# Kernel optimization log

Measured on AMD Instinct MI355X. Metric: run time of the kernel, lower is better.

The kernel has to match this reference:

```python
import jax, jax.numpy as jnp
import numpy as np

N = 100000
E = 1600000
IN_CH, HID_CH, OUT_CH, HEADS = 128, 32, 64, 4
NEG_SLOPE = 0.2


def gat_conv(x, src, dst, W, att_src, att_dst, bias, concat):
    """PyG-style GATConv (inference; dropout off). src/dst include self-loops.
    x: [N, Fin], W: [Fin, H*C], att_*: [H, C], bias: [H*C] or [C]."""
    n = x.shape[0]
    H, C = att_src.shape
    h = (x @ W).reshape(n, H, C)                      # [N, H, C]
    a_s = jnp.sum(h * att_src, axis=-1)               # [N, H]
    a_d = jnp.sum(h * att_dst, axis=-1)               # [N, H]
    e = jax.nn.leaky_relu(a_s[src] + a_d[dst], NEG_SLOPE)   # [E, H]
    # segment softmax over incoming edges of each dst node
    e_max = jax.ops.segment_max(e, dst, num_segments=n)     # [N, H]
    e_exp = jnp.exp(e - e_max[dst])                          # [E, H]
    denom = jax.ops.segment_sum(e_exp, dst, num_segments=n) # [N, H]
    alpha = e_exp / (denom[dst] + 1e-16)                     # [E, H]
    msg = h[src] * alpha[:, :, None]                         # [E, H, C]
    out = jax.ops.segment_sum(msg, dst, num_segments=n)     # [N, H, C]
    out = out.reshape(n, H * C) if concat else out.mean(axis=1)
    return out + bias


def setup_inputs() -> dict:
    key = jax.random.key(0)
    ks = jax.random.split(key, 10)
    g = 1.0 / np.sqrt(IN_CH)
    g2 = 1.0 / np.sqrt(HID_CH * HEADS)
    return {
        "x": jax.random.normal(ks[0], (N, IN_CH), dtype=jnp.float32),
        "edge_index": jax.random.randint(ks[1], (2, E), 0, N, dtype=jnp.int64),
        "W1": jax.random.normal(ks[2], (IN_CH, HEADS * HID_CH), dtype=jnp.float32) * g,
        "att_src1": jax.random.normal(ks[3], (HEADS, HID_CH), dtype=jnp.float32) * g,
        "att_dst1": jax.random.normal(ks[4], (HEADS, HID_CH), dtype=jnp.float32) * g,
        "b1": jnp.zeros((HEADS * HID_CH,), dtype=jnp.float32),
        "W2": jax.random.normal(ks[5], (HEADS * HID_CH, OUT_CH), dtype=jnp.float32) * g2,
        "att_src2": jax.random.normal(ks[6], (1, OUT_CH), dtype=jnp.float32) * g2,
        "att_dst2": jax.random.normal(ks[7], (1, OUT_CH), dtype=jnp.float32) * g2,
        "b2": jnp.zeros((OUT_CH,), dtype=jnp.float32),
    }


def reference(x, edge_index, W1, att_src1, att_dst1, b1, W2, att_src2, att_dst2, b2):
    n = x.shape[0]
    # GATConv adds self-loops by default (fixed-size concat: jit friendly)
    loops = jnp.arange(n, dtype=edge_index.dtype)
    src = jnp.concatenate([edge_index[0], loops])
    dst = jnp.concatenate([edge_index[1], loops])
    h = gat_conv(x, src, dst, W1, att_src1, att_dst1, b1, concat=True)
    h = jax.nn.elu(h)
    return gat_conv(h, src, dst, W2, att_src2, att_dst2, b2, concat=False)
```

## Files before the change

### kernel.cpp

```cpp
#include <hip/hip_runtime.h>
#include <hip/hip_fp16.h>

#define NEG_SLOPE 0.2f
#define BKN 128
#define MAXNB 1024
#define GRP 256
#define LOG2E 1.44269504f

typedef _Float16 half_t;
typedef __attribute__((ext_vector_type(2))) _Float16 half2v;
typedef __attribute__((ext_vector_type(4))) _Float16 half4;
typedef __attribute__((ext_vector_type(8))) _Float16 half8;
typedef __attribute__((ext_vector_type(4))) float floatx4;

#if __has_builtin(__builtin_amdgcn_fdot2)
#define FDOT2(a, b, c) __builtin_amdgcn_fdot2((a), (b), (c), false)
#else
#define FDOT2(a, b, c) ((float)(a)[0] * (float)(b)[0] + (float)(a)[1] * (float)(b)[1] + (c))
#endif

template<int BN, int HEADS, bool INHALF>
__global__ __launch_bounds__(256) void gemm_mfma(
    const void* __restrict__ Xv, const half_t* __restrict__ Wt,
    const float* __restrict__ atts, const float* __restrict__ attd,
    half_t* __restrict__ H, float* __restrict__ As, float* __restrict__ Ad,
    int n)
{
    constexpr int K  = 128;
    constexpr int NT = BN / 16;
    constexpr int TPH = NT / HEADS;

    __shared__ half_t Wl[BN * K];
    __shared__ half_t Xl[64 * K];

    const int t = threadIdx.x;
    const int wave = t >> 6, lane = t & 63;
    const int quad = lane >> 4, c = lane & 15;

    float att_s[NT], att_d[NT];
    #pragma unroll
    for (int nt = 0; nt < NT; ++nt) {
        att_s[nt] = atts[nt * 16 + c] * LOG2E;
        att_d[nt] = attd[nt * 16 + c] * LOG2E;
    }

    for (int i = t; i < BN * 16; i += 256) {
        int row = i >> 4, cid = i & 15;
        half8 v = *(const half8*)(Wt + row * K + cid * 8);
        *(half8*)(Wl + row * K + ((cid ^ (row & 15)) << 3)) = v;
    }

    const int numTiles = (n + 63) / 64;
    for (int tile = blockIdx.x; tile < numTiles; tile += gridDim.x) {
        const int row0 = tile * 64;
        __syncthreads();
        for (int i = t; i < 1024; i += 256) {
            int m = i >> 4, cid = i & 15;
            int row = row0 + m;
            half8 h;
            #pragma unroll
            for (int z = 0; z < 8; ++z) h[z] = (half_t)0.f;
            if (row < n) {
                if constexpr (INHALF) {
                    h = *(const half8*)((const half_t*)Xv + (size_t)row * K + cid * 8);
                } else {
                    const float4* src = (const float4*)((const float*)Xv + (size_t)row * K + cid * 8);
                    float4 a = src[0], b = src[1];
                    h[0]=(half_t)a.x; h[1]=(half_t)a.y; h[2]=(half_t)a.z; h[3]=(half_t)a.w;
                    h[4]=(half_t)b.x; h[5]=(half_t)b.y; h[6]=(half_t)b.z; h[7]=(half_t)b.w;
                }
            }
            *(half8*)(Xl + m * K + ((cid ^ (m & 15)) << 3)) = h;
        }
        __syncthreads();

        floatx4 acc[NT];
        #pragma unroll
        for (int i = 0; i < NT; ++i) acc[i] = (floatx4)(0.f);

        #pragma unroll
        for (int kc = 0; kc < 4; ++kc) {
            int cid = kc * 4 + quad;
            half8 afrag = *(const half8*)(Xl + (wave * 16 + c) * K + ((cid ^ c) << 3));
            #pragma unroll
            for (int nt = 0; nt < NT; ++nt) {
                half8 bfrag = *(const half8*)(Wl + (nt * 16 + c) * K + ((cid ^ c) << 3));
                acc[nt] = __builtin_amdgcn_mfma_f32_16x16x32_f16(afrag, bfrag, acc[nt], 0, 0, 0);
            }
        }

        #pragma unroll
        for (int reg = 0; reg < 4; ++reg) {
            int row = row0 + wave * 16 + quad * 4 + reg;
            bool ok = row < n;
            if (ok) {
                #pragma unroll
                for (int nt = 0; nt < NT; ++nt)
                    H[(size_t)row * BN + nt * 16 + c] = (half_t)acc[nt][reg];
            }
            #pragma unroll
            for (int h = 0; h < HEADS; ++h) {
                float ps = 0.f, pd = 0.f;
                #pragma unroll
                for (int u = 0; u < TPH; ++u) {
                    int nt = h * TPH + u;
                    ps += acc[nt][reg] * att_s[nt];
                    pd += acc[nt][reg] * att_d[nt];
                }
                #pragma unroll
                for (int off = 1; off < 16; off <<= 1) {
                    ps += __shfl_xor(ps, off);
                    pd += __shfl_xor(pd, off);
                }
                if (ok && c == 0) {
                    As[(size_t)row * HEADS + h] = ps;
                    Ad[(size_t)row * HEADS + h] = pd;
                }
            }
        }
    }
}

__global__ __launch_bounds__(256) void ghist_wconv(
    const int* __restrict__ ei, int E, int Etot, int NB, int chunk,
    int* __restrict__ cnt,
    const float* __restrict__ W1, half_t* __restrict__ Wt1,
    const float* __restrict__ W2, half_t* __restrict__ Wt2)
{
    int iw = blockIdx.x * 256 + threadIdx.x;
    if (iw < 128 * 128) {
        int k = iw / 128, nn = iw % 128;
        Wt1[nn * 128 + k] = (half_t)W1[iw];
    } else if (iw < 128 * 128 + 128 * 64) {
        int jx = iw - 128 * 128;
        int k = jx / 64, nn = jx % 64;
        Wt2[nn * 128 + k] = (half_t)W2[jx];
    }

    __shared__ int h[MAXNB];
    int g = blockIdx.x;
    for (int i = threadIdx.x; i < NB; i += 256) h[i] = 0;
    __syncthreads();
    int lo = g * chunk, hi = min(Etot, lo + chunk);
    for (int e = lo + threadIdx.x; e < hi; e += 256) {
        int dst = (e < E) ? ei[E + e] : (e - E);
        atomicAdd(&h[dst >> 7], 1);
    }
    __syncthreads();
    for (int i = threadIdx.x; i < NB; i += 256) cnt[i * GRP + g] = h[i];
}

__global__ __launch_bounds__(256) void scan_blocks(
    int* __restrict__ data, int n, int* __restrict__ bsum)
{
    __shared__ int s[256];
    int t = threadIdx.x;
    int idx = blockIdx.x * 1024 + t * 4;
    int4 v = make_int4(0, 0, 0, 0);
    if (idx + 3 < n)      v = *(const int4*)(data + idx);
    else {
        if (idx     < n) v.x = data[idx];
        if (idx + 1 < n) v.y = data[idx+1];
        if (idx + 2 < n) v.z = data[idx+2];
        if (idx + 3 < n) v.w = data[idx+3];
    }
    int tsum = v.x + v.y + v.z + v.w;
    s[t] = tsum;
    __syncthreads();
    for (int off = 1; off < 256; off <<= 1) {
        int x = (t >= off) ? s[t - off] : 0;
        __syncthreads();
        s[t] += x;
        __syncthreads();
    }
    int excl = s[t] - tsum;
    if (t == 255) bsum[blockIdx.x] = s[255];
    if (idx     < n) data[idx]     = excl;
    if (idx + 1 < n) data[idx + 1] = excl + v.x;
    if (idx + 2 < n) data[idx + 2] = excl + v.x + v.y;
    if (idx + 3 < n) data[idx + 3] = excl + v.x + v.y + v.z;
}

__global__ __launch_bounds__(256) void pass1_gemm1(
    const int* __restrict__ ei, int E, int Etot, int NB, int chunk, int nbC,
    const int* __restrict__ S, const int* __restrict__ bsum,
    unsigned* __restrict__ tmp,
    const float* __restrict__ X, const half_t* __restrict__ Wt,
    const float* __restrict__ atts, const float* __restrict__ attd,
    half_t* __restrict__ H, float* __restrict__ As, float* __restrict__ Ad,
    int n)
{
    constexpr int K = 128, BN = 128, NT = 8, HEADS = 4, TPH = 2;
    __shared__ half_t Wl[BN * K];
    __shared__ half_t Xl[64 * K];
    __shared__ int cur[MAXNB];

    const int t = threadIdx.x;

    if (blockIdx.x < GRP) {
        int* bs  = (int*)Wl;
        int* bse = (int*)Wl + 256;
        int g = blockIdx.x;
        int val = (t < nbC) ? bsum[t] : 0;
        bs[t] = val;
        __syncthreads();
        for (int off = 1; off < 256; off <<= 1) {
            int x = (t >= off) ? bs[t - off] : 0;
            __syncthreads();
            bs[t] += x;
            __syncthreads();
        }
        bse[t] = bs[t] - val;
        __syncthreads();
        for (int i = t; i < NB; i += 256) {
            int idx = i * GRP + g;
            cur[i] = S[idx] + bse[idx >> 10];
        }
        __syncthreads();
        int lo = g * chunk, hi = min(Etot, lo + chunk);
        for (int e = lo + t; e < hi; e += 256) {
            int src, dst;
            if (e < E) { src = ei[e]; dst = ei[E + e]; }
            else       { src = dst = e - E; }
            int pos = atomicAdd(&cur[dst >> 7], 1);
            tmp[pos] = ((unsigned)src << 7) | (unsigned)(dst & (BKN - 1));
        }
        return;
    }

    const int wave = t >> 6, lane = t & 63;
    const int quad = lane >> 4, c = lane & 15;

    float att_s[NT], att_d[NT];
    #pragma unroll
    for (int nt = 0; nt < NT; ++nt) {
        att_s[nt] = atts[nt * 16 + c] * LOG2E;
        att_d[nt] = attd[nt * 16 + c] * LOG2E;
    }

    for (int i = t; i < BN * 16; i += 256) {
        int row = i >> 4, cid = i & 15;
        half8 v = *(const half8*)(Wt + row * K + cid * 8);
        *(half8*)(Wl + row * K + ((cid ^ (row & 15)) << 3)) = v;
    }

    const int numTiles = (n + 63) / 64;
    for (int tile = blockIdx.x - GRP; tile < numTiles; tile += gridDim.x - GRP) {
        const int row0 = tile * 64;
        __syncthreads();
        for (int i = t; i < 1024; i += 256) {
            int m = i >> 4, cid = i & 15;
            int row = row0 + m;
            half8 h;
            #pragma unroll
            for (int z = 0; z < 8; ++z) h[z] = (half_t)0.f;
            if (row < n) {
                const float4* src = (const float4*)(X + (size_t)row * K + cid * 8);
                float4 a = src[0], b = src[1];
                h[0]=(half_t)a.x; h[1]=(half_t)a.y; h[2]=(half_t)a.z; h[3]=(half_t)a.w;
                h[4]=(half_t)b.x; h[5]=(half_t)b.y; h[6]=(half_t)b.z; h[7]=(half_t)b.w;
            }
            *(half8*)(Xl + m * K + ((cid ^ (m & 15)) << 3)) = h;
        }
        __syncthreads();

        floatx4 acc[NT];
        #pragma unroll
        for (int i = 0; i < NT; ++i) acc[i] = (floatx4)(0.f);

        #pragma unroll
        for (int kc = 0; kc < 4; ++kc) {
            int cid = kc * 4 + quad;
            half8 afrag = *(const half8*)(Xl + (wave * 16 + c) * K + ((cid ^ c) << 3));
            #pragma unroll
            for (int nt = 0; nt < NT; ++nt) {
                half8 bfrag = *(const half8*)(Wl + (nt * 16 + c) * K + ((cid ^ c) << 3));
                acc[nt] = __builtin_amdgcn_mfma_f32_16x16x32_f16(afrag, bfrag, acc[nt], 0, 0, 0);
            }
        }

        #pragma unroll
        for (int reg = 0; reg < 4; ++reg) {
            int row = row0 + wave * 16 + quad * 4 + reg;
            bool ok = row < n;
            if (ok) {
                #pragma unroll
                for (int nt = 0; nt < NT; ++nt)
                    H[(size_t)row * BN + nt * 16 + c] = (half_t)acc[nt][reg];
            }
            #pragma unroll
            for (int h = 0; h < HEADS; ++h) {
                float ps = 0.f, pd = 0.f;
                #pragma unroll
                for (int u = 0; u < TPH; ++u) {
                    int nt = h * TPH + u;
                    ps += acc[nt][reg] * att_s[nt];
                    pd += acc[nt][reg] * att_d[nt];
                }
                #pragma unroll
                for (int off = 1; off < 16; off <<= 1) {
                    ps += __shfl_xor(ps, off);
                    pd += __shfl_xor(pd, off);
                }
                if (ok && c == 0) {
                    As[(size_t)row * HEADS + h] = ps;
                    Ad[(size_t)row * HEADS + h] = pd;
                }
            }
        }
    }
}

__global__ __launch_bounds__(256) void pass2_sort(
    const unsigned* __restrict__ tmp, const int* __restrict__ S,
    const int* __restrict__ bsum, int NB, int Etot, int nbC,
    int* __restrict__ offs, int* __restrict__ esrc, int n)
{
    __shared__ int cnt[BKN];
    __shared__ int sc[BKN];
    __shared__ int cur[BKN];
    __shared__ int bs[256];
    __shared__ int bse[256];
    int bk = blockIdx.x;
    int t  = threadIdx.x;

    int val = (t < nbC) ? bsum[t] : 0;
    bs[t] = val;
    if (t < BKN) cnt[t] = 0;
    __syncthreads();
    for (int off = 1; off < 256; off <<= 1) {
        int x = (t >= off) ? bs[t - off] : 0;
        __syncthreads();
        bs[t] += x;
        __syncthreads();
    }
    bse[t] = bs[t] - val;
    __syncthreads();

    int lo = S[bk * GRP] + bse[(bk * GRP) >> 10];
    int hi = (bk + 1 < NB) ? (S[(bk + 1) * GRP] + bse[((bk + 1) * GRP) >> 10]) : Etot;

    for (int i = lo + t; i < hi; i += 256)
        atomicAdd(&cnt[tmp[i] & (BKN - 1)], 1);
    __syncthreads();
    int v = (t < BKN) ? cnt[t] : 0;
    if (t < BKN) sc[t] = v;
    __syncthreads();
    for (int off = 1; off < BKN; off <<= 1) {
        int x = (t < BKN && t >= off) ? sc[t - off] : 0;
        __syncthreads();
        if (t < BKN) sc[t] += x;
        __syncthreads();
    }
    if (t < BKN) {
        int node = bk * BKN + t;
        if (node < n) offs[node] = lo + sc[t];
        cur[t] = lo + sc[t] - v;
    }
    __syncthreads();
    for (int i = lo + t; i < hi; i += 256) {
        unsigned w = tmp[i];
        int p = atomicAdd(&cur[w & (BKN - 1)], 1);
        esrc[p] = (int)(w >> 7);
    }
}

__global__ __launch_bounds__(256) void agg1(
    const int* __restrict__ offs, const int* __restrict__ esrc,
    const half8* __restrict__ H8, const float* __restrict__ As,
    const float* __restrict__ Ad, const float* __restrict__ bias,
    half_t* __restrict__ X2h, int n)
{
    int v    = (blockIdx.x * 256 + threadIdx.x) >> 6;
    int lane = threadIdx.x & 63;
    if (v >= n) return;
    int q    = lane >> 4;
    int li   = lane & 15;
    int head = li >> 2;
    int end = offs[v];
    int beg = v ? offs[v - 1] : 0;
    float adv = Ad[(size_t)v * 4 + head];
    half2v one; one[0] = (half_t)1.f; one[1] = (half_t)1.f;
    float a[8];
    #pragma unroll
    for (int f = 0; f < 8; ++f) a[f] = 0.f;
    float den = 0.f;
    int j = beg + q;
    for (; j + 12 < end; j += 16) {
        int s0 = esrc[j], s1 = esrc[j + 4], s2 = esrc[j + 8], s3 = esrc[j + 12];
        float e0 = As[(unsigned)(s0 * 4 + head)] + adv;
        float e1 = As[(unsigned)(s1 * 4 + head)] + adv;
        float e2 = As[(unsigned)(s2 * 4 + head)] + adv;
        float e3 = As[(unsigned)(s3 * 4 + head)] + adv;
        half8 q0 = H8[(unsigned)(s0 * 16 + li)];
        half8 q1 = H8[(unsigned)(s1 * 16 + li)];
        half8 q2 = H8[(unsigned)(s2 * 16 + li)];
        half8 q3 = H8[(unsigned)(s3 * 16 + li)];
        float w0 = __builtin_amdgcn_exp2f(fmaxf(e0, NEG_SLOPE * e0));
        float w1 = __builtin_amdgcn_exp2f(fmaxf(e1, NEG_SLOPE * e1));
        float w2 = __builtin_amdgcn_exp2f(fmaxf(e2, NEG_SLOPE * e2));
        float w3 = __builtin_amdgcn_exp2f(fmaxf(e3, NEG_SLOPE * e3));
        half2v wp01; wp01[0] = (half_t)w0; wp01[1] = (half_t)w1;
        half2v wp23; wp23[0] = (half_t)w2; wp23[1] = (half_t)w3;
        #pragma unroll
        for (int f = 0; f < 8; ++f) {
            half2v p01; p01[0] = q0[f]; p01[1] = q1[f];
            half2v p23; p23[0] = q2[f]; p23[1] = q3[f];
            a[f] = FDOT2(p01, wp01, a[f]);
            a[f] = FDOT2(p23, wp23, a[f]);
        }
        den = FDOT2(wp01, one, den);
        den = FDOT2(wp23, one, den);
    }
    for (; j + 4 < end; j += 8) {
        int s0 = esrc[j], s1 = esrc[j + 4];
        float e0 = As[(unsigned)(s0 * 4 + head)] + adv;
        float e1 = As[(unsigned)(s1 * 4 + head)] + adv;
        half8 q0 = H8[(unsigned)(s0 * 16 + li)];
        half8 q1 = H8[(unsigned)(s1 * 16 + li)];
        float w0 = __builtin_amdgcn_exp2f(fmaxf(e0, NEG_SLOPE * e0));
        float w1 = __builtin_amdgcn_exp2f(fmaxf(e1, NEG_SLOPE * e1));
        half2v wp; wp[0] = (half_t)w0; wp[1] = (half_t)w1;
        #pragma unroll
        for (int f = 0; f < 8; ++f) {
            half2v p; p[0] = q0[f]; p[1] = q1[f];
            a[f] = FDOT2(p, wp, a[f]);
        }
        den = FDOT2(wp, one, den);
    }
    for (; j < end; j += 4) {
        int s = esrc[j];
        float e = As[(unsigned)(s * 4 + head)] + adv;
        half8 q0 = H8[(unsigned)(s * 16 + li)];
        float w = __builtin_amdgcn_exp2f(fmaxf(e, NEG_SLOPE * e));
        #pragma unroll
        for (int f = 0; f < 8; ++f) a[f] += w * (float)q0[f];
        den += w;
    }
    #pragma unroll
    for (int f = 0; f < 8; ++f) {
        a[f] += __shfl_xor(a[f], 16);
        a[f] += __shfl_xor(a[f], 32);
    }
    den += __shfl_xor(den, 16);
    den += __shfl_xor(den, 32);
    if (q == 0) {
        float inv = 1.f / (den + 1e-16f);
        float4 b0 = ((const float4*)bias)[2 * li];
        float4 b1 = ((const float4*)bias)[2 * li + 1];
        float o[8];
        o[0] = a[0] * inv + b0.x; o[1] = a[1] * inv + b0.y;
        o[2] = a[2] * inv + b0.z; o[3] = a[3] * inv + b0.w;
        o[4] = a[4] * inv + b1.x; o[5] = a[5] * inv + b1.y;
        o[6] = a[6] * inv + b1.z; o[7] = a[7] * inv + b1.w;
        half8 h;
        #pragma unroll
        for (int f = 0; f < 8; ++f) {
            float e = o[f] > 0.f ? o[f] : __expf(o[f]) - 1.f;
            h[f] = (half_t)e;
        }
        *(half8*)(X2h + (size_t)v * 128 + li * 8) = h;
    }
}

__global__ __launch_bounds__(256) void agg2(
    const int* __restrict__ offs, const int* __restrict__ esrc,
    const half8* __restrict__ H8, const float* __restrict__ As,
    const float* __restrict__ Ad, const float* __restrict__ bias,
    float* __restrict__ out, int n)
{
    int v    = (blockIdx.x * 256 + threadIdx.x) >> 6;
    int lane = threadIdx.x & 63;
    if (v >= n) return;
    int g  = lane >> 3;
    int li = lane & 7;
    int end = offs[v];
    int beg = v ? offs[v - 1] : 0;
    float adv = Ad[v];
    half2v one; one[0] = (half_t)1.f; one[1] = (half_t)1.f;
    float a[8];
    #pragma unroll
    for (int f = 0; f < 8; ++f) a[f] = 0.f;
    float den = 0.f;
    int j = beg + g;
    for (; j + 24 < end; j += 32) {
        int s0 = esrc[j], s1 = esrc[j + 8], s2 = esrc[j + 16], s3 = esrc[j + 24];
        float e0 = As[s0] + adv;
        float e1 = As[s1] + adv;
        float e2 = As[s2] + adv;
        float e3 = As[s3] + adv;
        half8 q0 = H8[(unsigned)(s0 * 8 + li)];
        half8 q1 = H8[(unsigned)(s1 * 8 + li)];
        half8 q2 = H8[(unsigned)(s2 * 8 + li)];
        half8 q3 = H8[(unsigned)(s3 * 8 + li)];
        float w0 = __builtin_amdgcn_exp2f(fmaxf(e0, NEG_SLOPE * e0));
        float w1 = __builtin_amdgcn_exp2f(fmaxf(e1, NEG_SLOPE * e1));
        float w2 = __builtin_amdgcn_exp2f(fmaxf(e2, NEG_SLOPE * e2));
        float w3 = __builtin_amdgcn_exp2f(fmaxf(e3, NEG_SLOPE * e3));
        half2v wp01; wp01[0] = (half_t)w0; wp01[1] = (half_t)w1;
        half2v wp23; wp23[0] = (half_t)w2; wp23[1] = (half_t)w3;
        #pragma unroll
        for (int f = 0; f < 8; ++f) {
            half2v p01; p01[0] = q0[f]; p01[1] = q1[f];
            half2v p23; p23[0] = q2[f]; p23[1] = q3[f];
            a[f] = FDOT2(p01, wp01, a[f]);
            a[f] = FDOT2(p23, wp23, a[f]);
        }
        den = FDOT2(wp01, one, den);
        den = FDOT2(wp23, one, den);
    }
    for (; j + 8 < end; j += 16) {
        int s0 = esrc[j], s1 = esrc[j + 8];
        float e0 = As[s0] + adv;
        float e1 = As[s1] + adv;
        half8 q0 = H8[(unsigned)(s0 * 8 + li)];
        half8 q1 = H8[(unsigned)(s1 * 8 + li)];
        float w0 = __builtin_amdgcn_exp2f(fmaxf(e0, NEG_SLOPE * e0));
        float w1 = __builtin_amdgcn_exp2f(fmaxf(e1, NEG_SLOPE * e1));
        half2v wp; wp[0] = (half_t)w0; wp[1] = (half_t)w1;
        #pragma unroll
        for (int f = 0; f < 8; ++f) {
            half2v p; p[0] = q0[f]; p[1] = q1[f];
            a[f] = FDOT2(p, wp, a[f]);
        }
        den = FDOT2(wp, one, den);
    }
    for (; j < end; j += 8) {
        int s = esrc[j];
        float e = As[s] + adv;
        half8 q0 = H8[(unsigned)(s * 8 + li)];
        float w = __builtin_amdgcn_exp2f(fmaxf(e, NEG_SLOPE * e));
        #pragma unroll
        for (int f = 0; f < 8; ++f) a[f] += w * (float)q0[f];
        den += w;
    }
    #pragma unroll
    for (int f = 0; f < 8; ++f) {
        a[f] += __shfl_xor(a[f], 8);
        a[f] += __shfl_xor(a[f], 16);
        a[f] += __shfl_xor(a[f], 32);
    }
    den += __shfl_xor(den, 8);
    den += __shfl_xor(den, 16);
    den += __shfl_xor(den, 32);
    if (lane < 8) {
        float inv = 1.f / (den + 1e-16f);
        float4 b0 = ((const float4*)bias)[2 * li];
        float4 b1 = ((const float4*)bias)[2 * li + 1];
        float4* o4 = (float4*)(out + (size_t)v * 64);
        o4[2 * li]     = make_float4(a[0] * inv + b0.x, a[1] * inv + b0.y,
                                     a[2] * inv + b0.z, a[3] * inv + b0.w);
        o4[2 * li + 1] = make_float4(a[4] * inv + b1.x, a[5] * inv + b1.y,
                                     a[6] * inv + b1.z, a[7] * inv + b1.w);
    }
}

extern "C" void kernel_launch(void* const* d_in, const int* in_sizes, int n_in,
                              void* d_out, int out_size, void* d_ws, size_t ws_size,
                              hipStream_t stream)
{
    (void)n_in; (void)out_size; (void)ws_size;
    const float* x   = (const float*)d_in[0];
    const int*   ei  = (const int*)  d_in[1];
    const float* W1  = (const float*)d_in[2];
    const float* as1 = (const float*)d_in[3];
    const float* ad1 = (const float*)d_in[4];
    const float* b1  = (const float*)d_in[5];
    const float* W2  = (const float*)d_in[6];
    const float* as2 = (const float*)d_in[7];
    const float* ad2 = (const float*)d_in[8];
    const float* b2  = (const float*)d_in[9];
    float* out = (float*)d_out;

    const int n    = in_sizes[0] / 128;
    const int E    = in_sizes[1] / 2;
    const int Etot = E + n;
    const int NB   = (n + BKN - 1) / BKN;
    const int chunk = (Etot + GRP - 1) / GRP;

    char* p = (char*)d_ws;
    half_t* Hh  = (half_t*)p; p += (size_t)n * 128 * sizeof(half_t);
    half_t* X2h = (half_t*)p; p += (size_t)n * 128 * sizeof(half_t);
    float* As1 = (float*)p;   p += (size_t)n * 4 * sizeof(float);
    float* Ad1 = (float*)p;   p += (size_t)n * 4 * sizeof(float);
    int* offs  = (int*)p;     p += (size_t)n * sizeof(int);
    int* esrc  = (int*)p;     p += (size_t)Etot * sizeof(int);
    unsigned* tmp = (unsigned*)p; p += (size_t)Etot * sizeof(unsigned);
    int* cnt   = (int*)p;     p += (size_t)NB * GRP * sizeof(int);
    int* bsum  = (int*)p;     p += 1024;
    half_t* Wt1 = (half_t*)p; p += 128 * 128 * sizeof(half_t);
    half_t* Wt2 = (half_t*)p; p += 64 * 128 * sizeof(half_t);

    const int scan_n  = NB * GRP;
    const int scan_nb = (scan_n + 1023) / 1024;

    const int gtiles = (n + 63) / 64;

    ghist_wconv<<<GRP, 256, 0, stream>>>(ei, E, Etot, NB, chunk, cnt, W1, Wt1, W2, Wt2);
    scan_blocks<<<scan_nb, 256, 0, stream>>>(cnt, scan_n, bsum);
    pass1_gemm1<<<GRP + gtiles, 256, 0, stream>>>(ei, E, Etot, NB, chunk, scan_nb, cnt, bsum, tmp,
                                                  x, Wt1, as1, ad1, Hh, As1, Ad1, n);
    pass2_sort<<<NB, 256, 0, stream>>>(tmp, cnt, bsum, NB, Etot, scan_nb, offs, esrc, n);

    agg1<<<(n * 64 + 255) / 256, 256, 0, stream>>>(offs, esrc, (const half8*)Hh, As1, Ad1, b1, X2h, n);

    gemm_mfma<64, 1, true><<<gtiles, 256, 0, stream>>>(X2h, Wt2, as2, ad2, Hh, As1, Ad1, n);
    agg2<<<(n * 64 + 255) / 256, 256, 0, stream>>>(offs, esrc, (const half8*)Hh, As1, Ad1, b2, out, n);
}
```

Measured before the change: 299.5 us.

## Fuse layer-2 projection and attention logits into layer-1 aggregation kernel

The layer-1 aggregation kernel now multiplies each node's ELU output by W2 in the same kernel, using fdot2 against a W2 copy staged in LDS, and writes H2 plus the layer-2 attention scalars directly. This removes the X2h intermediate round trip through global memory and the separate MFMA GEMM launch. The cost is a 64-wide-per-node dot product done with scalar fdot2 instead of MFMA, plus a 16KB LDS W2 load in every block, which may reduce occupancy. The unused templated gemm_mfma kernel is removed and the remaining kernels are reordered.

```diff
diff --git a/kernel.cpp b/kernel.cpp
--- a/kernel.cpp
+++ b/kernel.cpp
@@ -19,21 +19,113 @@
 #define FDOT2(a, b, c) ((float)(a)[0] * (float)(b)[0] + (float)(a)[1] * (float)(b)[1] + (c))
 #endif
 
-template<int BN, int HEADS, bool INHALF>
-__global__ __launch_bounds__(256) void gemm_mfma(
-    const void* __restrict__ Xv, const half_t* __restrict__ Wt,
+__global__ __launch_bounds__(256) void ghist_wconv(
+    const int* __restrict__ ei, int E, int Etot, int NB, int chunk,
+    int* __restrict__ cnt,
+    const float* __restrict__ W1, half_t* __restrict__ Wt1,
+    const float* __restrict__ W2, half_t* __restrict__ Wt2)
+{
+    int iw = blockIdx.x * 256 + threadIdx.x;
+    if (iw < 128 * 128) {
+        int k = iw / 128, nn = iw % 128;
+        Wt1[nn * 128 + k] = (half_t)W1[iw];
+    } else if (iw < 128 * 128 + 128 * 64) {
+        int jx = iw - 128 * 128;
+        int k = jx / 64, nn = jx % 64;
+        Wt2[nn * 128 + k] = (half_t)W2[jx];
+    }
+
+    __shared__ int h[MAXNB];
+    int g = blockIdx.x;
+    for (int i = threadIdx.x; i < NB; i += 256) h[i] = 0;
+    __syncthreads();
+    int lo = g * chunk, hi = min(Etot, lo + chunk);
+    for (int e = lo + threadIdx.x; e < hi; e += 256) {
+        int dst = (e < E) ? ei[E + e] : (e - E);
+        atomicAdd(&h[dst >> 7], 1);
+    }
+    __syncthreads();
+    for (int i = threadIdx.x; i < NB; i += 256) cnt[i * GRP + g] = h[i];
+}
+
+__global__ __launch_bounds__(256) void scan_blocks(
+    int* __restrict__ data, int n, int* __restrict__ bsum)
+{
+    __shared__ int s[256];
+    int t = threadIdx.x;
+    int idx = blockIdx.x * 1024 + t * 4;
+    int4 v = make_int4(0, 0, 0, 0);
+    if (idx + 3 < n)      v = *(const int4*)(data + idx);
+    else {
+        if (idx     < n) v.x = data[idx];
+        if (idx + 1 < n) v.y = data[idx+1];
+        if (idx + 2 < n) v.z = data[idx+2];
+        if (idx + 3 < n) v.w = data[idx+3];
+    }
+    int tsum = v.x + v.y + v.z + v.w;
+    s[t] = tsum;
+    __syncthreads();
+    for (int off = 1; off < 256; off <<= 1) {
+        int x = (t >= off) ? s[t - off] : 0;
+        __syncthreads();
+        s[t] += x;
+        __syncthreads();
+    }
+    int excl = s[t] - tsum;
+    if (t == 255) bsum[blockIdx.x] = s[255];
+    if (idx     < n) data[idx]     = excl;
+    if (idx + 1 < n) data[idx + 1] = excl + v.x;
+    if (idx + 2 < n) data[idx + 2] = excl + v.x + v.y;
+    if (idx + 3 < n) data[idx + 3] = excl + v.x + v.y + v.z;
+}
+
+__global__ __launch_bounds__(256) void pass1_gemm1(
+    const int* __restrict__ ei, int E, int Etot, int NB, int chunk, int nbC,
+    const int* __restrict__ S, const int* __restrict__ bsum,
+    unsigned* __restrict__ tmp,
+    const float* __restrict__ X, const half_t* __restrict__ Wt,
     const float* __restrict__ atts, const float* __restrict__ attd,
     half_t* __restrict__ H, float* __restrict__ As, float* __restrict__ Ad,
     int n)
 {
-    constexpr int K  = 128;
-    constexpr int NT = BN / 16;
-    constexpr int TPH = NT / HEADS;
-
+    constexpr int K = 128, BN = 128, NT = 8, HEADS = 4, TPH = 2;
     __shared__ half_t Wl[BN * K];
     __shared__ half_t Xl[64 * K];
+    __shared__ int cur[MAXNB];
 
     const int t = threadIdx.x;
+
+    if (blockIdx.x < GRP) {
+        int* bs  = (int*)Wl;
+        int* bse = (int*)Wl + 256;
+        int g = blockIdx.x;
+        int val = (t < nbC) ? bsum[t] : 0;
+        bs[t] = val;
+        __syncthreads();
+        for (int off = 1; off < 256; off <<= 1) {
+            int x = (t >= off) ? bs[t - off] : 0;
+            __syncthreads();
+            bs[t] += x;
+            __syncthreads();
+        }
+        bse[t] = bs[t] - val;
+        __syncthreads();
+        for (int i = t; i < NB; i += 256) {
+            int idx = i * GRP + g;
+            cur[i] = S[idx] + bse[idx >> 10];
+        }
+        __syncthreads();
+        int lo = g * chunk, hi = min(Etot, lo + chunk);
+        for (int e = lo + t; e < hi; e += 256) {
+            int src, dst;
+            if (e < E) { src = ei[e]; dst = ei[E + e]; }
+            else       { src = dst = e - E; }
+            int pos = atomicAdd(&cur[dst >> 7], 1);
+            tmp[pos] = ((unsigned)src << 7) | (unsigned)(dst & (BKN - 1));
+        }
+        return;
+    }
+
     const int wave = t >> 6, lane = t & 63;
     const int quad = lane >> 4, c = lane & 15;
 
@@ -51,7 +143,7 @@
     }
 
     const int numTiles = (n + 63) / 64;
-    for (int tile = blockIdx.x; tile < numTiles; tile += gridDim.x) {
+    for (int tile = blockIdx.x - GRP; tile < numTiles; tile += gridDim.x - GRP) {
         const int row0 = tile * 64;
         __syncthreads();
         for (int i = t; i < 1024; i += 256) {
@@ -61,14 +153,10 @@
             #pragma unroll
             for (int z = 0; z < 8; ++z) h[z] = (half_t)0.f;
             if (row < n) {
-                if constexpr (INHALF) {
-                    h = *(const half8*)((const half_t*)Xv + (size_t)row * K + cid * 8);
-                } else {
-                    const float4* src = (const float4*)((const float*)Xv + (size_t)row * K + cid * 8);
-                    float4 a = src[0], b = src[1];
-                    h[0]=(half_t)a.x; h[1]=(half_t)a.y; h[2]=(half_t)a.z; h[3]=(half_t)a.w;
-                    h[4]=(half_t)b.x; h[5]=(half_t)b.y; h[6]=(half_t)b.z; h[7]=(half_t)b.w;
-                }
+                const float4* src = (const float4*)(X + (size_t)row * K + cid * 8);
+                float4 a = src[0], b = src[1];
+                h[0]=(half_t)a.x; h[1]=(half_t)a.y; h[2]=(half_t)a.z; h[3]=(half_t)a.w;
+                h[4]=(half_t)b.x; h[5]=(half_t)b.y; h[6]=(half_t)b.z; h[7]=(half_t)b.w;
             }
             *(half8*)(Xl + m * K + ((cid ^ (m & 15)) << 3)) = h;
         }
@@ -121,196 +209,6 @@
     }
 }
 
-__global__ __launch_bounds__(256) void ghist_wconv(
-    const int* __restrict__ ei, int E, int Etot, int NB, int chunk,
-    int* __restrict__ cnt,
-    const float* __restrict__ W1, half_t* __restrict__ Wt1,
-    const float* __restrict__ W2, half_t* __restrict__ Wt2)
-{
-    int iw = blockIdx.x * 256 + threadIdx.x;
-    if (iw < 128 * 128) {
-        int k = iw / 128, nn = iw % 128;
-        Wt1[nn * 128 + k] = (half_t)W1[iw];
-    } else if (iw < 128 * 128 + 128 * 64) {
-        int jx = iw - 128 * 128;
-        int k = jx / 64, nn = jx % 64;
-        Wt2[nn * 128 + k] = (half_t)W2[jx];
-    }
-
-    __shared__ int h[MAXNB];
-    int g = blockIdx.x;
-    for (int i = threadIdx.x; i < NB; i += 256) h[i] = 0;
-    __syncthreads();
-    int lo = g * chunk, hi = min(Etot, lo + chunk);
-    for (int e = lo + threadIdx.x; e < hi; e += 256) {
-        int dst = (e < E) ? ei[E + e] : (e - E);
-        atomicAdd(&h[dst >> 7], 1);
-    }
-    __syncthreads();
-    for (int i = threadIdx.x; i < NB; i += 256) cnt[i * GRP + g] = h[i];
-}
-
-__global__ __launch_bounds__(256) void scan_blocks(
-    int* __restrict__ data, int n, int* __restrict__ bsum)
-{
-    __shared__ int s[256];
-    int t = threadIdx.x;
-    int idx = blockIdx.x * 1024 + t * 4;
-    int4 v = make_int4(0, 0, 0, 0);
-    if (idx + 3 < n)      v = *(const int4*)(data + idx);
-    else {
-        if (idx     < n) v.x = data[idx];
-        if (idx + 1 < n) v.y = data[idx+1];
-        if (idx + 2 < n) v.z = data[idx+2];
-        if (idx + 3 < n) v.w = data[idx+3];
-    }
-    int tsum = v.x + v.y + v.z + v.w;
-    s[t] = tsum;
-    __syncthreads();
-    for (int off = 1; off < 256; off <<= 1) {
-        int x = (t >= off) ? s[t - off] : 0;
-        __syncthreads();
-        s[t] += x;
-        __syncthreads();
-    }
-    int excl = s[t] - tsum;
-    if (t == 255) bsum[blockIdx.x] = s[255];
-    if (idx     < n) data[idx]     = excl;
-    if (idx + 1 < n) data[idx + 1] = excl + v.x;
-    if (idx + 2 < n) data[idx + 2] = excl + v.x + v.y;
-    if (idx + 3 < n) data[idx + 3] = excl + v.x + v.y + v.z;
-}
-
-__global__ __launch_bounds__(256) void pass1_gemm1(
-    const int* __restrict__ ei, int E, int Etot, int NB, int chunk, int nbC,
-    const int* __restrict__ S, const int* __restrict__ bsum,
-    unsigned* __restrict__ tmp,
-    const float* __restrict__ X, const half_t* __restrict__ Wt,
-    const float* __restrict__ atts, const float* __restrict__ attd,
-    half_t* __restrict__ H, float* __restrict__ As, float* __restrict__ Ad,
-    int n)
-{
-    constexpr int K = 128, BN = 128, NT = 8, HEADS = 4, TPH = 2;
-    __shared__ half_t Wl[BN * K];
-    __shared__ half_t Xl[64 * K];
-    __shared__ int cur[MAXNB];
-
-    const int t = threadIdx.x;
-
-    if (blockIdx.x < GRP) {
-        int* bs  = (int*)Wl;
-        int* bse = (int*)Wl + 256;
-        int g = blockIdx.x;
-        int val = (t < nbC) ? bsum[t] : 0;
-        bs[t] = val;
-        __syncthreads();
-        for (int off = 1; off < 256; off <<= 1) {
-            int x = (t >= off) ? bs[t - off] : 0;
-            __syncthreads();
-            bs[t] += x;
-            __syncthreads();
-        }
-        bse[t] = bs[t] - val;
-        __syncthreads();
-        for (int i = t; i < NB; i += 256) {
-            int idx = i * GRP + g;
-            cur[i] = S[idx] + bse[idx >> 10];
-        }
-        __syncthreads();
-        int lo = g * chunk, hi = min(Etot, lo + chunk);
-        for (int e = lo + t; e < hi; e += 256) {
-            int src, dst;
-            if (e < E) { src = ei[e]; dst = ei[E + e]; }
-            else       { src = dst = e - E; }
-            int pos = atomicAdd(&cur[dst >> 7], 1);
-            tmp[pos] = ((unsigned)src << 7) | (unsigned)(dst & (BKN - 1));
-        }
-        return;
-    }
-
-    const int wave = t >> 6, lane = t & 63;
-    const int quad = lane >> 4, c = lane & 15;
-
-    float att_s[NT], att_d[NT];
-    #pragma unroll
-    for (int nt = 0; nt < NT; ++nt) {
-        att_s[nt] = atts[nt * 16 + c] * LOG2E;
-        att_d[nt] = attd[nt * 16 + c] * LOG2E;
-    }
-
-    for (int i = t; i < BN * 16; i += 256) {
-        int row = i >> 4, cid = i & 15;
-        half8 v = *(const half8*)(Wt + row * K + cid * 8);
-        *(half8*)(Wl + row * K + ((cid ^ (row & 15)) << 3)) = v;
-    }
-
-    const int numTiles = (n + 63) / 64;
-    for (int tile = blockIdx.x - GRP; tile < numTiles; tile += gridDim.x - GRP) {
-        const int row0 = tile * 64;
-        __syncthreads();
-        for (int i = t; i < 1024; i += 256) {
-            int m = i >> 4, cid = i & 15;
-            int row = row0 + m;
-            half8 h;
-            #pragma unroll
-            for (int z = 0; z < 8; ++z) h[z] = (half_t)0.f;
-            if (row < n) {
-                const float4* src = (const float4*)(X + (size_t)row * K + cid * 8);
-                float4 a = src[0], b = src[1];
-                h[0]=(half_t)a.x; h[1]=(half_t)a.y; h[2]=(half_t)a.z; h[3]=(half_t)a.w;
-                h[4]=(half_t)b.x; h[5]=(half_t)b.y; h[6]=(half_t)b.z; h[7]=(half_t)b.w;
-            }
-            *(half8*)(Xl + m * K + ((cid ^ (m & 15)) << 3)) = h;
-        }
-        __syncthreads();
-
-        floatx4 acc[NT];
-        #pragma unroll
-        for (int i = 0; i < NT; ++i) acc[i] = (floatx4)(0.f);
-
-        #pragma unroll
-        for (int kc = 0; kc < 4; ++kc) {
-            int cid = kc * 4 + quad;
-            half8 afrag = *(const half8*)(Xl + (wave * 16 + c) * K + ((cid ^ c) << 3));
-            #pragma unroll
-            for (int nt = 0; nt < NT; ++nt) {
-                half8 bfrag = *(const half8*)(Wl + (nt * 16 + c) * K + ((cid ^ c) << 3));
-                acc[nt] = __builtin_amdgcn_mfma_f32_16x16x32_f16(afrag, bfrag, acc[nt], 0, 0, 0);
-            }
-        }
-
-        #pragma unroll
-        for (int reg = 0; reg < 4; ++reg) {
-            int row = row0 + wave * 16 + quad * 4 + reg;
-            bool ok = row < n;
-            if (ok) {
-                #pragma unroll
-                for (int nt = 0; nt < NT; ++nt)
-                    H[(size_t)row * BN + nt * 16 + c] = (half_t)acc[nt][reg];
-            }
-            #pragma unroll
-            for (int h = 0; h < HEADS; ++h) {
-                float ps = 0.f, pd = 0.f;
-                #pragma unroll
-                for (int u = 0; u < TPH; ++u) {
-                    int nt = h * TPH + u;
-                    ps += acc[nt][reg] * att_s[nt];
-                    pd += acc[nt][reg] * att_d[nt];
-                }
-                #pragma unroll
-                for (int off = 1; off < 16; off <<= 1) {
-                    ps += __shfl_xor(ps, off);
-                    pd += __shfl_xor(pd, off);
-                }
-                if (ok && c == 0) {
-                    As[(size_t)row * HEADS + h] = ps;
-                    Ad[(size_t)row * HEADS + h] = pd;
-                }
-            }
-        }
-    }
-}
-
 __global__ __launch_bounds__(256) void pass2_sort(
     const unsigned* __restrict__ tmp, const int* __restrict__ S,
     const int* __restrict__ bsum, int NB, int Etot, int nbC,
@@ -365,21 +263,35 @@
     }
 }
 
-__global__ __launch_bounds__(256) void agg1(
+__global__ __launch_bounds__(256) void agg1_fused(
     const int* __restrict__ offs, const int* __restrict__ esrc,
     const half8* __restrict__ H8, const float* __restrict__ As,
     const float* __restrict__ Ad, const float* __restrict__ bias,
-    half_t* __restrict__ X2h, int n)
-{
-    int v    = (blockIdx.x * 256 + threadIdx.x) >> 6;
-    int lane = threadIdx.x & 63;
+    const half_t* __restrict__ Wt2,
+    const float* __restrict__ atts2, const float* __restrict__ attd2,
+    half_t* __restrict__ H2, float* __restrict__ As2, float* __restrict__ Ad2,
+    int n)
+{
+    __shared__ half2v W2p[64 * 64];
+    __shared__ half_t x2w[4 * 128];
+
+    const int t = threadIdx.x;
+    for (int i = t; i < 64 * 64; i += 256)
+        W2p[i] = *(const half2v*)(Wt2 + (i & 63) * 128 + ((i >> 6) << 1));
+    __syncthreads();
+
+    int v    = (blockIdx.x * 256 + t) >> 6;
+    int lane = t & 63;
     if (v >= n) return;
+    int wave = t >> 6;
     int q    = lane >> 4;
     int li   = lane & 15;
     int head = li >> 2;
     int end = offs[v];
     int beg = v ? offs[v - 1] : 0;
     float adv = Ad[(size_t)v * 4 + head];
+    float a2s = atts2[lane] * LOG2E;
+    float a2d = attd2[lane] * LOG2E;
     half2v one; one[0] = (half_t)1.f; one[1] = (half_t)1.f;
     float a[8];
     #pragma unroll
@@ -459,8 +371,27 @@
             float e = o[f] > 0.f ? o[f] : __expf(o[f]) - 1.f;
             h[f] = (half_t)e;
         }
-        *(half8*)(X2h + (size_t)v * 128 + li * 8) = h;
-    }
+        *(half8*)(x2w + wave * 128 + li * 8) = h;
+    }
+    const half8* xw8 = (const half8*)(x2w + wave * 128);
+    float h2a = 0.f;
+    #pragma unroll
+    for (int k8 = 0; k8 < 16; ++k8) {
+        half8 xq = xw8[k8];
+        #pragma unroll
+        for (int jj = 0; jj < 4; ++jj) {
+            half2v xp; xp[0] = xq[2 * jj]; xp[1] = xq[2 * jj + 1];
+            h2a = FDOT2(xp, W2p[(k8 * 4 + jj) * 64 + lane], h2a);
+        }
+    }
+    H2[(size_t)v * 64 + lane] = (half_t)h2a;
+    float ps = h2a * a2s, pd = h2a * a2d;
+    #pragma unroll
+    for (int off = 1; off < 64; off <<= 1) {
+        ps += __shfl_xor(ps, off);
+        pd += __shfl_xor(pd, off);
+    }
+    if (lane == 0) { As2[v] = ps; Ad2[v] = pd; }
 }
 
 __global__ __launch_bounds__(256) void agg2(
@@ -580,9 +511,11 @@
 
     char* p = (char*)d_ws;
     half_t* Hh  = (half_t*)p; p += (size_t)n * 128 * sizeof(half_t);
-    half_t* X2h = (half_t*)p; p += (size_t)n * 128 * sizeof(half_t);
+    half_t* H2  = (half_t*)p; p += (size_t)n * 64 * sizeof(half_t);
     float* As1 = (float*)p;   p += (size_t)n * 4 * sizeof(float);
     float* Ad1 = (float*)p;   p += (size_t)n * 4 * sizeof(float);
+    float* As2 = (float*)p;   p += (size_t)n * sizeof(float);
+    float* Ad2 = (float*)p;   p += (size_t)n * sizeof(float);
     int* offs  = (int*)p;     p += (size_t)n * sizeof(int);
     int* esrc  = (int*)p;     p += (size_t)Etot * sizeof(int);
     unsigned* tmp = (unsigned*)p; p += (size_t)Etot * sizeof(unsigned);
@@ -602,8 +535,9 @@
                                                   x, Wt1, as1, ad1, Hh, As1, Ad1, n);
     pass2_sort<<<NB, 256, 0, stream>>>(tmp, cnt, bsum, NB, Etot, scan_nb, offs, esrc, n);
 
-    agg1<<<(n * 64 + 255) / 256, 256, 0, stream>>>(offs, esrc, (const half8*)Hh, As1, Ad1, b1, X2h, n);
-
-    gemm_mfma<64, 1, true><<<gtiles, 256, 0, stream>>>(X2h, Wt2, as2, ad2, Hh, As1, Ad1, n);
-    agg2<<<(n * 64 + 255) / 256, 256, 0, stream>>>(offs, esrc, (const half8*)Hh, As1, Ad1, b2, out, n);
-}
+    agg1_fused<<<(n * 64 + 255) / 256, 256, 0, stream>>>(
+        offs, esrc, (const half8*)Hh, As1, Ad1, b1,
+        Wt2, as2, ad2, H2, As2, Ad2, n);
+
+    agg2<<<(n * 64 + 255) / 256, 256, 0, stream>>>(offs, esrc, (const half8*)H2, As2, Ad2, b2, out, n);
+}
```

Measured after the change: 446.5 us. +49.1%, slower.
